# Kernel tuning notes

Hardware: AMD Instinct MI355X
Metric: run time of the kernel (lower is better)

Reference implementation:

```python
import jax, jax.numpy as jnp
import numpy as np


def setup_inputs() -> dict:
    key = jax.random.key(0)
    k1, k2 = jax.random.split(key)
    B, C, H, W = 64, 64, 64, 64
    map1 = jax.random.normal(k1, (B, C, H, W), dtype=jnp.float32)
    map2 = jax.random.normal(k2, (B, C, H, W), dtype=jnp.float32)
    return {"map1": map1, "map2": map2}


def reference(map1, map2):
    # conv2d(map1, map2) with equal spatial dims -> [B,B,1,1]; .diag() keeps
    # only the per-sample full cross-correlation: c_i = sum(map1[i]*map2[i]).
    corr = jnp.einsum('bchw,bchw->b', map1, map2)          # [B]
    corr = corr / jnp.linalg.norm(corr)                    # L2-normalize over batch
    corr = 1.0 - corr
    # out[i] = map1[i] + map2[i] * corr[i]
    return map1 + map2 * corr[:, None, None, None]
```

## Files before the change

### kernel.cpp

```cpp
#include <hip/hip_runtime.h>


#define THREADS 256
#define NBATCH 64
#define BPB 64
#define V4B 65536
#define V4BLK 1024

__global__ __launch_bounds__(THREADS, 8) void corr_reduce_kernel(
    const float4* __restrict__ m1, const float4* __restrict__ m2,
    float* __restrict__ partials) {
  const int b = blockIdx.y;
  const int base = b * V4B + blockIdx.x * V4BLK + threadIdx.x;

  float4 a[4], v[4];
#pragma unroll
  for (int k = 0; k < 4; ++k) a[k] = m1[base + k * THREADS];
#pragma unroll
  for (int k = 0; k < 4; ++k) v[k] = m2[base + k * THREADS];
  __builtin_amdgcn_sched_barrier(0);

  float acc0 = 0.f, acc1 = 0.f, acc2 = 0.f, acc3 = 0.f;
#pragma unroll
  for (int k = 0; k < 4; ++k) {
    acc0 = fmaf(a[k].x, v[k].x, acc0);
    acc1 = fmaf(a[k].y, v[k].y, acc1);
    acc2 = fmaf(a[k].z, v[k].z, acc2);
    acc3 = fmaf(a[k].w, v[k].w, acc3);
  }
  float acc = (acc0 + acc1) + (acc2 + acc3);

#pragma unroll
  for (int off = 32; off > 0; off >>= 1) acc += __shfl_xor(acc, off);

  __shared__ float wsum[4];
  if ((threadIdx.x & 63) == 0) wsum[threadIdx.x >> 6] = acc;
  __syncthreads();
  if (threadIdx.x == 0)
    partials[b * BPB + blockIdx.x] = (wsum[0] + wsum[1]) + (wsum[2] + wsum[3]);
}

__global__ __launch_bounds__(THREADS, 4) void corr_apply_kernel(
    const float4* __restrict__ m1, const float4* __restrict__ m2,
    const float4* __restrict__ partials4, float4* __restrict__ out) {
  const int b = blockIdx.y;
  const int base = b * V4B + blockIdx.x * V4BLK + threadIdx.x;

  float4 a[4], v[4];
#pragma unroll
  for (int k = 0; k < 4; ++k) a[k] = m1[base + k * THREADS];
#pragma unroll
  for (int k = 0; k < 4; ++k) v[k] = m2[base + k * THREADS];

  float4 p[4];
#pragma unroll
  for (int k = 0; k < 4; ++k) p[k] = partials4[threadIdx.x * 4 + k];
  __builtin_amdgcn_sched_barrier(0);

  float s = 0.f;
#pragma unroll
  for (int k = 0; k < 4; ++k) s += (p[k].x + p[k].y) + (p[k].z + p[k].w);
  s += __shfl_xor(s, 1);
  s += __shfl_xor(s, 2);

  __shared__ float csh[NBATCH];
  __shared__ float c_sh;
  if ((threadIdx.x & 3) == 0) csh[threadIdx.x >> 2] = s;
  __syncthreads();
  if (threadIdx.x < 64) {
    float cv = csh[threadIdx.x];
    float sq = cv * cv;
#pragma unroll
    for (int off = 32; off > 0; off >>= 1) sq += __shfl_xor(sq, off);
    if (threadIdx.x == 0) c_sh = 1.0f - csh[b] * rsqrtf(sq);
  }
  __syncthreads();
  const float c = c_sh;

#pragma unroll
  for (int k = 0; k < 4; ++k) {
    float4 o;
    o.x = fmaf(v[k].x, c, a[k].x);
    o.y = fmaf(v[k].y, c, a[k].y);
    o.z = fmaf(v[k].z, c, a[k].z);
    o.w = fmaf(v[k].w, c, a[k].w);
    out[base + k * THREADS] = o;
  }
}

extern "C" void kernel_launch(void* const* d_in, const int* in_sizes, int n_in,
                              void* d_out, int out_size, void* d_ws, size_t ws_size,
                              hipStream_t stream) {
  const float4* m1 = (const float4*)d_in[0];
  const float4* m2 = (const float4*)d_in[1];
  float* partials = (float*)d_ws;
  float4* out = (float4*)d_out;

  dim3 grid(BPB, NBATCH);
  corr_reduce_kernel<<<grid, THREADS, 0, stream>>>(m1, m2, partials);
  corr_apply_kernel<<<grid, THREADS, 0, stream>>>(m1, m2, (const float4*)partials, out);
}
```

Measured before the change: 184.0 us.

## Stream segments through double-buffered LDS with global_load_lds in both kernels

Each block now covers a 4096-float4 segment instead of 1024, so there are 16 blocks per batch instead of 64. Both the reduce and the apply kernel stream their inputs through a two-slot LDS buffer, filled by direct global-to-LDS loads and paced with manual vmcnt waits, so loads stay in flight while compute runs. The apply kernel also computes the normalization factor within a single wave using shuffles, which removes the shared-memory handoff and the block barriers. The risks are fewer, longer-running blocks giving less latency hiding across waves, and hand-written waitcnt values that must exactly match the mix of loads and stores in flight.

```diff
diff --git a/kernel.cpp b/kernel.cpp
--- a/kernel.cpp
+++ b/kernel.cpp
@@ -3,88 +3,112 @@
 
 #define THREADS 256
 #define NBATCH 64
-#define BPB 64
+#define BPB 16
 #define V4B 65536
-#define V4BLK 1024
+#define V4SEG 4096
 
-__global__ __launch_bounds__(THREADS, 8) void corr_reduce_kernel(
+typedef const __attribute__((address_space(1))) void* gptr_t;
+typedef __attribute__((address_space(3))) void* lptr_t;
+
+__device__ __forceinline__ void stage(const float4* __restrict__ m1,
+                                      const float4* __restrict__ m2,
+                                      float4* lds4, int segBase, int i) {
+  const int t = threadIdx.x;
+  const int w64 = t & ~63;
+  const int sb = (i & 1) * 1024;
+  const int k0 = 2 * i;
+  __builtin_amdgcn_global_load_lds((gptr_t)&m1[segBase + (k0 + 0) * 256 + t],
+                                   (lptr_t)&lds4[sb + 0 * 256 + w64], 16, 0, 0);
+  __builtin_amdgcn_global_load_lds((gptr_t)&m1[segBase + (k0 + 1) * 256 + t],
+                                   (lptr_t)&lds4[sb + 1 * 256 + w64], 16, 0, 0);
+  __builtin_amdgcn_global_load_lds((gptr_t)&m2[segBase + (k0 + 0) * 256 + t],
+                                   (lptr_t)&lds4[sb + 2 * 256 + w64], 16, 0, 0);
+  __builtin_amdgcn_global_load_lds((gptr_t)&m2[segBase + (k0 + 1) * 256 + t],
+                                   (lptr_t)&lds4[sb + 3 * 256 + w64], 16, 0, 0);
+}
+
+__global__ __launch_bounds__(THREADS, 4) void corr_reduce_kernel(
     const float4* __restrict__ m1, const float4* __restrict__ m2,
     float* __restrict__ partials) {
+  __shared__ float4 lds4[2048];
+  __shared__ float wsum[4];
+  const int t = threadIdx.x;
   const int b = blockIdx.y;
-  const int base = b * V4B + blockIdx.x * V4BLK + threadIdx.x;
+  const int segBase = b * V4B + blockIdx.x * V4SEG;
 
-  float4 a[4], v[4];
-#pragma unroll
-  for (int k = 0; k < 4; ++k) a[k] = m1[base + k * THREADS];
-#pragma unroll
-  for (int k = 0; k < 4; ++k) v[k] = m2[base + k * THREADS];
-  __builtin_amdgcn_sched_barrier(0);
+  stage(m1, m2, lds4, segBase, 0);
+  stage(m1, m2, lds4, segBase, 1);
 
   float acc0 = 0.f, acc1 = 0.f, acc2 = 0.f, acc3 = 0.f;
 #pragma unroll
-  for (int k = 0; k < 4; ++k) {
-    acc0 = fmaf(a[k].x, v[k].x, acc0);
-    acc1 = fmaf(a[k].y, v[k].y, acc1);
-    acc2 = fmaf(a[k].z, v[k].z, acc2);
-    acc3 = fmaf(a[k].w, v[k].w, acc3);
+  for (int i = 0; i < 8; ++i) {
+    if (i < 7) asm volatile("s_waitcnt vmcnt(4)" ::: "memory");
+    else       asm volatile("s_waitcnt vmcnt(0)" ::: "memory");
+    __builtin_amdgcn_sched_barrier(0);
+    const int sb = (i & 1) * 1024;
+    const float4 a0 = lds4[sb + t];
+    const float4 a1 = lds4[sb + 256 + t];
+    const float4 v0 = lds4[sb + 512 + t];
+    const float4 v1 = lds4[sb + 768 + t];
+    acc0 = fmaf(a0.x, v0.x, acc0); acc1 = fmaf(a0.y, v0.y, acc1);
+    acc2 = fmaf(a0.z, v0.z, acc2); acc3 = fmaf(a0.w, v0.w, acc3);
+    acc0 = fmaf(a1.x, v1.x, acc0); acc1 = fmaf(a1.y, v1.y, acc1);
+    acc2 = fmaf(a1.z, v1.z, acc2); acc3 = fmaf(a1.w, v1.w, acc3);
+    if (i < 6) stage(m1, m2, lds4, segBase, i + 2);
   }
   float acc = (acc0 + acc1) + (acc2 + acc3);
 
 #pragma unroll
   for (int off = 32; off > 0; off >>= 1) acc += __shfl_xor(acc, off);
-
-  __shared__ float wsum[4];
-  if ((threadIdx.x & 63) == 0) wsum[threadIdx.x >> 6] = acc;
+  if ((t & 63) == 0) wsum[t >> 6] = acc;
   __syncthreads();
-  if (threadIdx.x == 0)
+  if (t == 0)
     partials[b * BPB + blockIdx.x] = (wsum[0] + wsum[1]) + (wsum[2] + wsum[3]);
 }
 
 __global__ __launch_bounds__(THREADS, 4) void corr_apply_kernel(
     const float4* __restrict__ m1, const float4* __restrict__ m2,
     const float4* __restrict__ partials4, float4* __restrict__ out) {
+  __shared__ float4 lds4[2048];
+  const int t = threadIdx.x;
+  const int lane = t & 63;
   const int b = blockIdx.y;
-  const int base = b * V4B + blockIdx.x * V4BLK + threadIdx.x;
+  const int segBase = b * V4B + blockIdx.x * V4SEG;
 
-  float4 a[4], v[4];
-#pragma unroll
-  for (int k = 0; k < 4; ++k) a[k] = m1[base + k * THREADS];
-#pragma unroll
-  for (int k = 0; k < 4; ++k) v[k] = m2[base + k * THREADS];
-
-  float4 p[4];
-#pragma unroll
-  for (int k = 0; k < 4; ++k) p[k] = partials4[threadIdx.x * 4 + k];
-  __builtin_amdgcn_sched_barrier(0);
+  stage(m1, m2, lds4, segBase, 0);
+  stage(m1, m2, lds4, segBase, 1);
 
   float s = 0.f;
 #pragma unroll
-  for (int k = 0; k < 4; ++k) s += (p[k].x + p[k].y) + (p[k].z + p[k].w);
-  s += __shfl_xor(s, 1);
-  s += __shfl_xor(s, 2);
-
-  __shared__ float csh[NBATCH];
-  __shared__ float c_sh;
-  if ((threadIdx.x & 3) == 0) csh[threadIdx.x >> 2] = s;
-  __syncthreads();
-  if (threadIdx.x < 64) {
-    float cv = csh[threadIdx.x];
-    float sq = cv * cv;
+  for (int j = 0; j < 4; ++j) {
+    const float4 p = partials4[4 * lane + j];
+    s += (p.x + p.y) + (p.z + p.w);
+  }
+  float sq = s * s;
 #pragma unroll
-    for (int off = 32; off > 0; off >>= 1) sq += __shfl_xor(sq, off);
-    if (threadIdx.x == 0) c_sh = 1.0f - csh[b] * rsqrtf(sq);
-  }
-  __syncthreads();
-  const float c = c_sh;
+  for (int off = 32; off > 0; off >>= 1) sq += __shfl_xor(sq, off);
+  const float cb = __shfl(s, b);
+  const float c = 1.0f - cb * rsqrtf(sq);
 
 #pragma unroll
-  for (int k = 0; k < 4; ++k) {
-    float4 o;
-    o.x = fmaf(v[k].x, c, a[k].x);
-    o.y = fmaf(v[k].y, c, a[k].y);
-    o.z = fmaf(v[k].z, c, a[k].z);
-    o.w = fmaf(v[k].w, c, a[k].w);
-    out[base + k * THREADS] = o;
+  for (int i = 0; i < 8; ++i) {
+    if (i < 7) asm volatile("s_waitcnt vmcnt(6)" ::: "memory");
+    else       asm volatile("s_waitcnt vmcnt(2)" ::: "memory");
+    __builtin_amdgcn_sched_barrier(0);
+    const int sb = (i & 1) * 1024;
+    const int k0 = 2 * i;
+    const float4 a0 = lds4[sb + t];
+    const float4 a1 = lds4[sb + 256 + t];
+    const float4 v0 = lds4[sb + 512 + t];
+    const float4 v1 = lds4[sb + 768 + t];
+    float4 o0, o1;
+    o0.x = fmaf(v0.x, c, a0.x); o0.y = fmaf(v0.y, c, a0.y);
+    o0.z = fmaf(v0.z, c, a0.z); o0.w = fmaf(v0.w, c, a0.w);
+    o1.x = fmaf(v1.x, c, a1.x); o1.y = fmaf(v1.y, c, a1.y);
+    o1.z = fmaf(v1.z, c, a1.z); o1.w = fmaf(v1.w, c, a1.w);
+    out[segBase + (k0 + 0) * 256 + t] = o0;
+    out[segBase + (k0 + 1) * 256 + t] = o1;
+    if (i < 6) stage(m1, m2, lds4, segBase, i + 2);
   }
 }
 
@@ -98,5 +122,6 @@
 
   dim3 grid(BPB, NBATCH);
   corr_reduce_kernel<<<grid, THREADS, 0, stream>>>(m1, m2, partials);
-  corr_apply_kernel<<<grid, THREADS, 0, stream>>>(m1, m2, (const float4*)partials, out);
+  corr_apply_kernel<<<grid, THREADS, 0, stream>>>(m1, m2,
+                                                  (const float4*)partials, out);
 }
```

After: 190.3 us. 3.4% more time.
